# Kernel tuning notes

Measured on AMD Instinct MI355X. Metric: run time of the kernel, lower is better.

The kernel has to match this reference:

```python
import jax, jax.numpy as jnp
import numpy as np

B, S, I, E, NH, HID, L = 32, 512, 64, 128, 8, 1024, 4
HD = E // NH
TEMP = 0.05
EPS_BN = 1e-5
EPS_LN = 1e-5


def _pe(seq_len, d_model):
    # sinusoidal positional encoding, matches PositionalEncoding buffer pe[:seq_len, 0, :]
    pos = jnp.arange(seq_len, dtype=jnp.float32)[:, None]
    div = jnp.exp(jnp.arange(0, d_model, 2, dtype=jnp.float32) * (-np.log(10000.0) / d_model))
    pe = jnp.zeros((seq_len, d_model), jnp.float32)
    pe = pe.at[:, 0::2].set(jnp.sin(pos * div))
    pe = pe.at[:, 1::2].set(jnp.cos(pos * div))
    return pe


def _bn(x, g, b, axis):
    # eval-mode BatchNorm1d with running_mean=0, running_var=1 (affine scale+shift)
    sh = [1] * x.ndim
    sh[axis] = -1
    return x * (g / jnp.sqrt(1.0 + EPS_BN)).reshape(sh) + b.reshape(sh)


def _ln(x, g, b):
    m = jnp.mean(x, axis=-1, keepdims=True)
    v = jnp.var(x, axis=-1, keepdims=True)
    return (x - m) / jnp.sqrt(v + EPS_LN) * g + b


def _layer(h, Wqkv, bqkv, Wo, bo, g1, b1, g2, b2, W1, bf1, W2, bf2):
    # h: (S, B, E); post-LN torch TransformerEncoderLayer, relu FFN
    s, b = h.shape[0], h.shape[1]
    qkv = h @ Wqkv + bqkv                                  # (S, B, 3E)
    q, k, v = jnp.split(qkv, 3, axis=-1)
    sp = lambda t: t.reshape(s, b, NH, HD).transpose(1, 2, 0, 3)  # (B, NH, S, HD)
    q, k, v = sp(q), sp(k), sp(v)
    att = jax.nn.softmax(jnp.einsum('bhqd,bhkd->bhqk', q, k) * (1.0 / np.sqrt(HD)), axis=-1)
    o = jnp.einsum('bhqk,bhkd->bhqd', att, v).transpose(2, 0, 1, 3).reshape(s, b, E)
    h = _ln(h + o @ Wo + bo, g1, b1)
    ff = jax.nn.relu(h @ W1 + bf1) @ W2 + bf2
    h = _ln(h + ff, g2, b2)
    return h, att.mean(axis=1)  # attn averaged over heads: (B, S, S)


def setup_inputs() -> dict:
    key = jax.random.key(0)
    ks = iter(jax.random.split(key, 64))
    r = lambda *sh: jax.random.normal(next(ks), sh, jnp.float32) * 0.02
    return dict(
        x=jax.random.normal(next(ks), (B, S, I), jnp.float32),
        Wt=r(I, E), bt=r(E),
        bn1_g=jnp.ones(E), bn1_b=jnp.zeros(E),
        bn2_g=jnp.ones(E), bn2_b=jnp.zeros(E),
        Wqkv=r(L, E, 3 * E), bqkv=r(L, 3 * E), Wo=r(L, E, E), bo=r(L, E),
        ln1_g=jnp.ones((L, E)), ln1_b=jnp.zeros((L, E)),
        ln2_g=jnp.ones((L, E)), ln2_b=jnp.zeros((L, E)),
        W1=r(L, E, HID), b1=r(L, HID), W2=r(L, HID, E), b2=r(L, E),
        bn3_g=jnp.ones(E), bn3_b=jnp.zeros(E),
        Wd=r(E, I), bd=r(I), bn4_g=jnp.ones(I), bn4_b=jnp.zeros(I),
        Ws=r(S, HID), bs=r(HID), bn5_g=jnp.ones(HID), bn5_b=jnp.zeros(HID),
        Wtext=r(1024, HID), btext=r(HID), lnT_g=jnp.ones(HID), lnT_b=jnp.zeros(HID),
        sensor_emb=jax.random.normal(next(ks), (I, 1024), jnp.float32),
    )


def reference(x, Wt, bt, bn1_g, bn1_b, bn2_g, bn2_b,
              Wqkv, bqkv, Wo, bo, ln1_g, ln1_b, ln2_g, ln2_b,
              W1, b1, W2, b2, bn3_g, bn3_b,
              Wd, bd, bn4_g, bn4_b, Ws, bs, bn5_g, bn5_b,
              Wtext, btext, lnT_g, lnT_b, sensor_emb):
    # trunk_net: Linear -> BN(E) -> PE -> BN(E)
    h = x @ Wt + bt                                  # (B, S, E)
    h = _bn(h.transpose(0, 2, 1), bn1_g, bn1_b, 1)   # (B, E, S)
    h = h.transpose(2, 0, 1)                         # (S, B, E)
    h = h + _pe(h.shape[0], E)[:, None, :]
    h = _bn(h.transpose(1, 2, 0), bn2_g, bn2_b, 1)   # (B, E, S)
    h = h.transpose(2, 0, 1)                         # (S, B, E)
    for i in range(L):
        h, attn = _layer(h, Wqkv[i], bqkv[i], Wo[i], bo[i],
                         ln1_g[i], ln1_b[i], ln2_g[i], ln2_b[i],
                         W1[i], b1[i], W2[i], b2[i])
    h = _bn(h.transpose(1, 2, 0), bn3_g, bn3_b, 1)   # (B, E, S)
    # downsample_embedding_to_input_net
    d = jax.nn.relu(h.transpose(0, 2, 1) @ Wd + bd)  # (B, S, I)
    d = _bn(d.transpose(0, 2, 1), bn4_g, bn4_b, 1)   # (B, I, S)
    # sequence_representation_net
    imu = jax.nn.relu(d @ Ws + bs)                   # (B, I, HID)
    imu = _bn(imu, bn5_g, bn5_b, 2)
    # text_to_shared_net on sensor embeddings
    sens = _ln(jax.nn.relu(sensor_emb @ Wtext + btext), lnT_g, lnT_b)  # (I, HID)
    # fused pairwise cosine similarity (torch expands to (B,I,I,HID); we don't)
    imu_n = imu / jnp.maximum(jnp.linalg.norm(imu, axis=-1, keepdims=True), 1e-8)
    sens_n = sens / jnp.maximum(jnp.linalg.norm(sens, axis=-1, keepdims=True), 1e-8)
    return jnp.einsum('bih,jh->bij', imu_n, sens_n) / TEMP  # (B, I, I)
```

## Files before the change

### kernel.cpp

```cpp
#include <hip/hip_runtime.h>
#include <hip/hip_bf16.h>

#define B_   32
#define S_   512
#define I_   64
#define E_   128
#define NH_  8
#define HD_  16
#define HID_ 1024
#define L_   4
#define NTOK (B_*S_)

typedef __hip_bfloat16 bf16;
typedef __attribute__((ext_vector_type(8))) short bf16x8;
typedef __attribute__((ext_vector_type(4))) short bf16x4;
typedef __attribute__((ext_vector_type(4))) float f32x4;

__device__ __forceinline__ float b2f(bf16 v) { return __bfloat162float(v); }

template<bool F32>
__device__ __forceinline__ float ld(const void* p, size_t i) {
    if (F32) return ((const float*)p)[i];
    return b2f(((const bf16*)p)[i]);
}

__device__ __forceinline__ unsigned short f2bu(float f) {
    union { bf16 h; unsigned short u; } c; c.h = __float2bfloat16(f); return c.u;
}
__device__ __forceinline__ unsigned short b2u(bf16 h) {
    union { bf16 h; unsigned short u; } c; c.h = h; return c.u;
}
__device__ __forceinline__ float u2f(unsigned short u) {
    return __uint_as_float((unsigned int)u << 16);
}

__global__ void k_flag(const void* bn1g, int* flag) {
    if (threadIdx.x == 0) {
        const unsigned short* u = (const unsigned short*)bn1g;
        int zeros = 0;
        for (int i = 0; i < 32; ++i) zeros += (u[i] == 0);
        flag[0] = (zeros >= 8) ? 1 : 0;
    }
}

struct TrJobs {
    const void* in[7];
    bf16*       out[7];
    int R[7];
    int C[7];
    int start[8];
};

template<bool F32>
__device__ void tr_all_body(const TrJobs& j, float (*tile)[33])
{
    int bid = blockIdx.x;
    int job = 0;
#pragma unroll
    for (int t = 0; t < 6; ++t) if (bid >= j.start[t + 1]) job = t + 1;
    int local = bid - j.start[job];
    int R = j.R[job], C = j.C[job];
    int nx = C >> 5, ny = R >> 5;
    int per_z = nx * ny;
    int z = local / per_z;
    int rem = local - z * per_z;
    int cy = rem / nx, cx = rem - cy * nx;
    const void* in = j.in[job];
    bf16* out = j.out[job];

    size_t off = (size_t)z * R * C;
    int c0 = cx * 32, r0 = cy * 32;
    int tx = threadIdx.x;
    for (int i = threadIdx.y; i < 32; i += 8)
        tile[i][tx] = ld<F32>(in, off + (size_t)(r0 + i) * C + c0 + tx);
    __syncthreads();
    for (int i = threadIdx.y; i < 32; i += 8)
        out[off + (size_t)(c0 + i) * R + r0 + tx] = __float2bfloat16(tile[tx][i]);
}
__global__ __launch_bounds__(256) void k_tr_all(TrJobs j, const int* flag)
{
    __shared__ float tile[32][33];
    if (*flag) tr_all_body<true>(j, tile);
    else       tr_all_body<false>(j, tile);
}

struct PkJobs {
    const bf16* in[5];
    bf16*       out[5];
    int K[5];
    int NT[5];
    int KT[5];
    int start[6];
};

__global__ __launch_bounds__(256) void k_pack(PkJobs j)
{
    int fb = blockIdx.x * 4 + (threadIdx.x >> 6);
    if (fb >= j.start[5]) return;
    int lane = threadIdx.x & 63;
    int job = 0;
#pragma unroll
    for (int t = 0; t < 4; ++t) if (fb >= j.start[t + 1]) job = t + 1;
    int local = fb - j.start[job];
    int K = j.K[job], NT = j.NT[job], KT = j.KT[job];
    int per_z = NT * KT;
    int z = local / per_z;
    int rem = local - z * per_z;
    int ct = rem / KT, kt = rem - ct * KT;
    int l15 = lane & 15, quad = lane >> 4;
    const bf16* in = j.in[job] + (size_t)z * NT * 16 * K;
    bf16* out = j.out[job] + (size_t)z * per_z * 512 + (size_t)(ct * KT + kt) * 512 + lane * 8;
    *(uint4*)out = *(const uint4*)&in[(size_t)(ct * 16 + l15) * K + kt * 32 + quad * 8];
}

template<bool F32>
__device__ void trunk_body(const void* x, const void* Wt, const void* bt,
                           const void* g1, const void* c1,
                           const void* g2, const void* c2, float* __restrict__ h,
                           float (*xs)[I_])
{
    const int TOK = 8;
    int t0 = blockIdx.x * TOK;
    int tid = threadIdx.x;
    for (int idx = tid; idx < TOK * I_; idx += 128) {
        int tt = idx >> 6, k = idx & 63;
        xs[tt][k] = ld<F32>(x, (size_t)(t0 + tt) * I_ + k);
    }
    __syncthreads();
    int e = tid;
    float acc[TOK];
    float bias = ld<F32>(bt, e);
#pragma unroll
    for (int tt = 0; tt < TOK; ++tt) acc[tt] = bias;
    for (int k = 0; k < I_; ++k) {
        float w = ld<F32>(Wt, k * E_ + e);
#pragma unroll
        for (int tt = 0; tt < TOK; ++tt) acc[tt] += xs[tt][k] * w;
    }
    float rs = rsqrtf(1.0f + 1e-5f);
    float a1 = ld<F32>(g1, e) * rs, d1 = ld<F32>(c1, e);
    float a2 = ld<F32>(g2, e) * rs, d2 = ld<F32>(c2, e);
    int p = e >> 1;
    float freq = __expf(-(float)p * 0.14391157f);
#pragma unroll
    for (int tt = 0; tt < TOK; ++tt) {
        int t = t0 + tt;
        int s = t & (S_ - 1);
        float ang = (float)s * freq;
        float pe = (e & 1) ? cosf(ang) : sinf(ang);
        float v = acc[tt] * a1 + d1 + pe;
        h[(size_t)t * E_ + e] = v * a2 + d2;
    }
}
__global__ __launch_bounds__(128) void k_trunk(
    const void* x, const void* Wt, const void* bt,
    const void* g1, const void* c1, const void* g2, const void* c2,
    float* h, const int* flag)
{
    __shared__ float xs[8][I_];
    if (*flag) trunk_body<true>(x, Wt, bt, g1, c1, g2, c2, h, xs);
    else       trunk_body<false>(x, Wt, bt, g1, c1, g2, c2, h, xs);
}

template<bool F32>
__device__ void qkvm_body(const float* __restrict__ h, const bf16* __restrict__ WP,
                          const void* bias, size_t obi, bf16* __restrict__ qkv,
                          unsigned short (*A_s)[136])
{
    int t0 = blockIdx.x * 32;
    int tid = threadIdx.x;
    int wv = tid >> 6, lane = tid & 63;
    int l15 = lane & 15, quad = lane >> 4;

    {
        const float4* h4 = (const float4*)(h + (size_t)t0 * E_);
        for (int i = tid; i < 32 * E_ / 4; i += 256) {
            float4 v = h4[i];
            int row = i >> 5, col = (i & 31) * 4;
            unsigned int w0 = (unsigned int)f2bu(v.x) | ((unsigned int)f2bu(v.y) << 16);
            unsigned int w1 = (unsigned int)f2bu(v.z) | ((unsigned int)f2bu(v.w) << 16);
            *(uint2*)&A_s[row][col] = (uint2){w0, w1};
        }
    }
    __syncthreads();

    bf16x8 af[2][4];
#pragma unroll
    for (int kt = 0; kt < 4; ++kt) {
        int k0 = kt * 32 + quad * 8;
        af[0][kt] = *(const bf16x8*)&A_s[l15][k0];
        af[1][kt] = *(const bf16x8*)&A_s[16 + l15][k0];
    }
    for (int nt = 0; nt < 6; ++nt) {
        int col = wv * 96 + nt * 16 + l15;
        int ct = wv * 6 + nt;
        f32x4 acc0 = {0.f, 0.f, 0.f, 0.f}, acc1 = {0.f, 0.f, 0.f, 0.f};
#pragma unroll
        for (int kt = 0; kt < 4; ++kt) {
            bf16x8 bfr = *(const bf16x8*)&WP[(size_t)((ct * 4 + kt) * 64 + lane) * 8];
            acc0 = __builtin_amdgcn_mfma_f32_16x16x32_bf16(af[0][kt], bfr, acc0, 0, 0, 0);
            acc1 = __builtin_amdgcn_mfma_f32_16x16x32_bf16(af[1][kt], bfr, acc1, 0, 0, 0);
        }
        float bb = ld<F32>(bias, obi + col);
#pragma unroll
        for (int r = 0; r < 4; ++r) {
            qkv[(size_t)(t0 + quad * 4 + r) * 384 + col]      = __float2bfloat16(acc0[r] + bb);
            qkv[(size_t)(t0 + 16 + quad * 4 + r) * 384 + col] = __float2bfloat16(acc1[r] + bb);
        }
    }
}
__global__ __launch_bounds__(256) void k_qkv(
    const float* h, const bf16* WP, const void* bias, size_t obi,
    bf16* qkv, const int* flag)
{
    __shared__ unsigned short A_s[32][136];
    if (*flag) qkvm_body<true>(h, WP, bias, obi, qkv, A_s);
    else       qkvm_body<false>(h, WP, bias, obi, qkv, A_s);
}

__global__ __launch_bounds__(512) void k_attn(bf16* qkv)
{
    __shared__ unsigned short Ks[S_ * 16];
    __shared__ unsigned short Qs[256 * 16];
    __shared__ unsigned short VT[HD_ * 520];

    int bx = blockIdx.x;
    int qh = bx & 1;
    int hh = (bx >> 1) & (NH_ - 1);
    int b  = bx >> 4;
    int tid = threadIdx.x;
    const size_t base = (size_t)(b * S_) * 384 + hh * HD_;
    const float qs = 0.25f * 1.44269504f;

    for (int i = tid; i < S_ * 2; i += 512) {
        int s = i >> 1, hf = i & 1;
        uint4 v = *(const uint4*)(qkv + base + (size_t)s * 384 + 128 + hf * 8);
        unsigned int* w = (unsigned int*)&v;
#pragma unroll
        for (int j = 0; j < 4; ++j) {
            unsigned int lo = f2bu(u2f((unsigned short)(w[j] & 0xffff)) * qs);
            unsigned int hi = f2bu(u2f((unsigned short)(w[j] >> 16)) * qs);
            w[j] = lo | (hi << 16);
        }
        *(uint4*)&Ks[s * 16 + hf * 8] = v;
    }
    for (int i = tid; i < 256 * 2; i += 512) {
        int s = i >> 1, hf = i & 1;
        *(uint4*)&Qs[s * 16 + hf * 8] =
            *(const uint4*)(qkv + base + (size_t)(qh * 256 + s) * 384 + hf * 8);
    }
    {
        int s = tid;
        uint4 v0 = *(const uint4*)(qkv + base + (size_t)s * 384 + 256);
        uint4 v1 = *(const uint4*)(qkv + base + (size_t)s * 384 + 256 + 8);
        const unsigned short* u0 = (const unsigned short*)&v0;
        const unsigned short* u1 = (const unsigned short*)&v1;
#pragma unroll
        for (int dd = 0; dd < 8; ++dd) VT[dd * 520 + s] = u0[dd];
#pragma unroll
        for (int dd = 0; dd < 8; ++dd) VT[(8 + dd) * 520 + s] = u1[dd];
    }
    __syncthreads();

    int wv = tid >> 6, lane = tid & 63;
    int l15 = lane & 15, quad = lane >> 4;
    const f32x4 z4 = {0.f, 0.f, 0.f, 0.f};

    bf16x4 bq0 = *(const bf16x4*)&Qs[(wv * 32 + l15) * 16 + quad * 4];
    bf16x4 bq1 = *(const bf16x4*)&Qs[(wv * 32 + 16 + l15) * 16 + quad * 4];

    f32x4 O0 = z4, O1 = z4;
    float den0 = 0.f, den1 = 0.f;

#pragma unroll 2
    for (int kt = 0; kt < 32; ++kt) {
        bf16x4 ak = *(const bf16x4*)&Ks[(kt * 16 + l15) * 16 + quad * 4];
        bf16x4 av = *(const bf16x4*)&VT[l15 * 520 + kt * 16 + quad * 4];

        f32x4 s0 = __builtin_amdgcn_mfma_f32_16x16x16bf16_1k(ak, bq0, z4, 0, 0, 0);
        f32x4 s1 = __builtin_amdgcn_mfma_f32_16x16x16bf16_1k(ak, bq1, z4, 0, 0, 0);

        float p0[4], p1[4];
#pragma unroll
        for (int r = 0; r < 4; ++r) { p0[r] = exp2f(s0[r]); den0 += p0[r]; }
#pragma unroll
        for (int r = 0; r < 4; ++r) { p1[r] = exp2f(s1[r]); den1 += p1[r]; }

        bf16x4 pa0, pa1;
#pragma unroll
        for (int r = 0; r < 4; ++r) { pa0[r] = (short)f2bu(p0[r]); pa1[r] = (short)f2bu(p1[r]); }

        O0 = __builtin_amdgcn_mfma_f32_16x16x16bf16_1k(av, pa0, O0, 0, 0, 0);
        O1 = __builtin_amdgcn_mfma_f32_16x16x16bf16_1k(av, pa1, O1, 0, 0, 0);
    }

    den0 += __shfl_xor(den0, 16, 64);
    den0 += __shfl_xor(den0, 32, 64);
    den1 += __shfl_xor(den1, 16, 64);
    den1 += __shfl_xor(den1, 32, 64);
    float inv0 = 1.0f / den0;
    float inv1 = 1.0f / den1;

    int q0 = qh * 256 + wv * 32 + l15;
    bf16* out0 = qkv + (size_t)(b * S_ + q0) * 384 + hh * HD_ + quad * 4;
    bf16* out1 = out0 + (size_t)16 * 384;
    unsigned int a0 = (unsigned int)f2bu(O0[0] * inv0) | ((unsigned int)f2bu(O0[1] * inv0) << 16);
    unsigned int a1 = (unsigned int)f2bu(O0[2] * inv0) | ((unsigned int)f2bu(O0[3] * inv0) << 16);
    *(uint2*)out0 = (uint2){a0, a1};
    unsigned int c0 = (unsigned int)f2bu(O1[0] * inv1) | ((unsigned int)f2bu(O1[1] * inv1) << 16);
    unsigned int c1 = (unsigned int)f2bu(O1[2] * inv1) | ((unsigned int)f2bu(O1[3] * inv1) << 16);
    *(uint2*)out1 = (uint2){c0, c1};
}

#define FTOK 32
#define APAD 8
#define MHALF 512
#define MPAD 8

template<bool F32>
__device__ void projffn_body(const bf16* __restrict__ qkv, const bf16* __restrict__ WoP,
                             const void* bo, size_t obo,
                             const void* g1, const void* be1,
                             const bf16* __restrict__ W1P, const void* b1, size_t ob1,
                             const bf16* __restrict__ W2P, const void* b2v, size_t ob2,
                             const void* g2, const void* be2, size_t oln,
                             float* __restrict__ h,
                             const bf16* __restrict__ WqP, const void* bqv, size_t obq,
                             bf16* __restrict__ qkvout,
                             const bf16* __restrict__ WdP, const void* bd,
                             const void* g3, const void* c3,
                             const void* g4, const void* c4,
                             float* __restrict__ dbuf, int mode,
                             unsigned short (*A_s)[E_ + APAD],
                             unsigned short (*mid_s)[MHALF + MPAD],
                             float (*red)[32][2])
{
    int t0 = blockIdx.x * FTOK;
    int tid = threadIdx.x;
    int wv = tid >> 6, lane = tid & 63;
    int l15 = lane & 15, quad = lane >> 4;
    int c0 = wv * 16 + l15;

    {
        int row = tid >> 4, seg = tid & 15;
        *(uint4*)&A_s[row][seg * 8] =
            *(const uint4*)&qkv[(size_t)(t0 + row) * 384 + seg * 8];
    }
    __syncthreads();

    bf16x8 af[2][4];
#pragma unroll
    for (int kt = 0; kt < 4; ++kt) {
        int k0 = kt * 32 + quad * 8;
        af[0][kt] = *(const bf16x8*)&A_s[l15][k0];
        af[1][kt] = *(const bf16x8*)&A_s[16 + l15][k0];
    }
    f32x4 acc[2];
    acc[0] = (f32x4){0.f, 0.f, 0.f, 0.f};
    acc[1] = (f32x4){0.f, 0.f, 0.f, 0.f};
#pragma unroll
    for (int kt = 0; kt < 4; ++kt) {
        bf16x8 bb0 = *(const bf16x8*)&WoP[(size_t)((wv * 4 + kt) * 64 + lane) * 8];
        acc[0] = __builtin_amdgcn_mfma_f32_16x16x32_bf16(af[0][kt], bb0, acc[0], 0, 0, 0);
        acc[1] = __builtin_amdgcn_mfma_f32_16x16x32_bf16(af[1][kt], bb0, acc[1], 0, 0, 0);
    }

    float bo0 = ld<F32>(bo, obo + c0);
    float val[2][4], s1[2][4], s2[2][4];
#pragma unroll
    for (int mt = 0; mt < 2; ++mt) {
#pragma unroll
        for (int r = 0; r < 4; ++r) {
            size_t row = (size_t)(t0 + mt * 16 + quad * 4 + r);
            float v0 = acc[mt][r] + bo0 + h[row * E_ + c0];
            val[mt][r] = v0;
            s1[mt][r] = v0;
            s2[mt][r] = v0 * v0;
        }
    }
#pragma unroll
    for (int off = 1; off < 16; off <<= 1) {
#pragma unroll
        for (int mt = 0; mt < 2; ++mt)
#pragma unroll
            for (int r = 0; r < 4; ++r) {
                s1[mt][r] += __shfl_xor(s1[mt][r], off, 64);
                s2[mt][r] += __shfl_xor(s2[mt][r], off, 64);
            }
    }
    if (l15 == 0) {
#pragma unroll
        for (int mt = 0; mt < 2; ++mt)
#pragma unroll
            for (int r = 0; r < 4; ++r) {
                red[wv][mt * 16 + quad * 4 + r][0] = s1[mt][r];
                red[wv][mt * 16 + quad * 4 + r][1] = s2[mt][r];
            }
    }
    __syncthreads();

    float val1[2][4];
    {
        float g10 = ld<F32>(g1, oln + c0);
        float b10 = ld<F32>(be1, oln + c0);
#pragma unroll
        for (int mt = 0; mt < 2; ++mt) {
#pragma unroll
            for (int r = 0; r < 4; ++r) {
                int rw = mt * 16 + quad * 4 + r;
                float su = red[0][rw][0] + red[1][rw][0] + red[2][rw][0] + red[3][rw][0]
                         + red[4][rw][0] + red[5][rw][0] + red[6][rw][0] + red[7][rw][0];
                float sq = red[0][rw][1] + red[1][rw][1] + red[2][rw][1] + red[3][rw][1]
                         + red[4][rw][1] + red[5][rw][1] + red[6][rw][1] + red[7][rw][1];
                float mean = su * (1.0f / E_);
                float var = fmaxf(sq * (1.0f / E_) - mean * mean, 0.0f);
                float rstd = rsqrtf(var + 1e-5f);
                float h0 = (val[mt][r] - mean) * rstd * g10 + b10;
                val1[mt][r] = h0;
                A_s[rw][c0] = f2bu(h0);
            }
        }
    }
    __syncthreads();

    bf16x8 af1[2][4];
#pragma unroll
    for (int kt = 0; kt < 4; ++kt) {
        int k0 = kt * 32 + quad * 8;
        af1[0][kt] = *(const bf16x8*)&A_s[l15][k0];
        af1[1][kt] = *(const bf16x8*)&A_s[16 + l15][k0];
    }

    f32x4 acc2[2];
    acc2[0] = (f32x4){0.f, 0.f, 0.f, 0.f};
    acc2[1] = (f32x4){0.f, 0.f, 0.f, 0.f};

    for (int p = 0; p < 2; ++p) {
        for (int nt = 0; nt < 4; ++nt) {
            int col = p * MHALF + wv * 64 + nt * 16 + l15;
            int lc  = wv * 64 + nt * 16 + l15;
            int ct  = p * 32 + wv * 4 + nt;
            f32x4 acc0 = {0.f, 0.f, 0.f, 0.f}, acc1 = {0.f, 0.f, 0.f, 0.f};
#pragma unroll
            for (int kt = 0; kt < 4; ++kt) {
                bf16x8 bfr = *(const bf16x8*)&W1P[(size_t)((ct * 4 + kt) * 64 + lane) * 8];
                acc0 = __builtin_amdgcn_mfma_f32_16x16x32_bf16(af1[0][kt], bfr, acc0, 0, 0, 0);
                acc1 = __builtin_amdgcn_mfma_f32_16x16x32_bf16(af1[1][kt], bfr, acc1, 0, 0, 0);
            }
            float bias = ld<F32>(b1, ob1 + col);
#pragma unroll
            for (int r = 0; r < 4; ++r) {
                mid_s[quad * 4 + r][lc]      = f2bu(fmaxf(acc0[r] + bias, 0.f));
                mid_s[16 + quad * 4 + r][lc] = f2bu(fmaxf(acc1[r] + bias, 0.f));
            }
        }
        __syncthreads();

        for (int kk = 0; kk < 16; ++kk) {
            int kt = p * 16 + kk;
            int k0l = kk * 32 + quad * 8;
            bf16x8 a0 = *(const bf16x8*)&mid_s[l15][k0l];
            bf16x8 a1 = *(const bf16x8*)&mid_s[16 + l15][k0l];
            bf16x8 bb0 = *(const bf16x8*)&W2P[(size_t)((wv * 32 + kt) * 64 + lane) * 8];
            acc2[0] = __builtin_amdgcn_mfma_f32_16x16x32_bf16(a0, bb0, acc2[0], 0, 0, 0);
            acc2[1] = __builtin_amdgcn_mfma_f32_16x16x32_bf16(a1, bb0, acc2[1], 0, 0, 0);
        }
        __syncthreads();
    }

    float b20 = ld<F32>(b2v, ob2 + c0);
#pragma unroll
    for (int mt = 0; mt < 2; ++mt) {
#pragma unroll
        for (int r = 0; r < 4; ++r) {
            float v0 = acc2[mt][r] + b20 + val1[mt][r];
            val[mt][r] = v0;
            s1[mt][r] = v0;
            s2[mt][r] = v0 * v0;
        }
    }
#pragma unroll
    for (int off = 1; off < 16; off <<= 1) {
#pragma unroll
        for (int mt = 0; mt < 2; ++mt)
#pragma unroll
            for (int r = 0; r < 4; ++r) {
                s1[mt][r] += __shfl_xor(s1[mt][r], off, 64);
                s2[mt][r] += __shfl_xor(s2[mt][r], off, 64);
            }
    }
    if (l15 == 0) {
#pragma unroll
        for (int mt = 0; mt < 2; ++mt)
#pragma unroll
            for (int r = 0; r < 4; ++r) {
                red[wv][mt * 16 + quad * 4 + r][0] = s1[mt][r];
                red[wv][mt * 16 + quad * 4 + r][1] = s2[mt][r];
            }
    }
    __syncthreads();
    float g20 = ld<F32>(g2, oln + c0);
    float be20 = ld<F32>(be2, oln + c0);
    float rsb = rsqrtf(1.0f + 1e-5f);
    float a3 = (mode == 2) ? ld<F32>(g3, c0) * rsb : 0.f;
    float d3 = (mode == 2) ? ld<F32>(c3, c0) : 0.f;
#pragma unroll
    for (int mt = 0; mt < 2; ++mt) {
#pragma unroll
        for (int r = 0; r < 4; ++r) {
            int rw = mt * 16 + quad * 4 + r;
            float su = red[0][rw][0] + red[1][rw][0] + red[2][rw][0] + red[3][rw][0]
                     + red[4][rw][0] + red[5][rw][0] + red[6][rw][0] + red[7][rw][0];
            float sq = red[0][rw][1] + red[1][rw][1] + red[2][rw][1] + red[3][rw][1]
                     + red[4][rw][1] + red[5][rw][1] + red[6][rw][1] + red[7][rw][1];
            float mean = su * (1.0f / E_);
            float var = fmaxf(sq * (1.0f / E_) - mean * mean, 0.0f);
            float rstd = rsqrtf(var + 1e-5f);
            size_t row = (size_t)(t0 + rw);
            float outv = (val[mt][r] - mean) * rstd * g20 + be20;
            if (mode != 2) {
                h[row * E_ + c0] = outv;
                A_s[rw][c0] = f2bu(outv);
            } else {
                A_s[rw][c0] = f2bu(outv * a3 + d3);
            }
        }
    }

    if (mode == 1) {
        __syncthreads();
        bf16x8 afq[2][4];
#pragma unroll
        for (int kt = 0; kt < 4; ++kt) {
            int k0 = kt * 32 + quad * 8;
            afq[0][kt] = *(const bf16x8*)&A_s[l15][k0];
            afq[1][kt] = *(const bf16x8*)&A_s[16 + l15][k0];
        }
        for (int nt = 0; nt < 3; ++nt) {
            int ct = wv * 3 + nt;
            int col = ct * 16 + l15;
            f32x4 q0 = {0.f, 0.f, 0.f, 0.f}, q1 = {0.f, 0.f, 0.f, 0.f};
#pragma unroll
            for (int kt = 0; kt < 4; ++kt) {
                bf16x8 bfr = *(const bf16x8*)&WqP[(size_t)((ct * 4 + kt) * 64 + lane) * 8];
                q0 = __builtin_amdgcn_mfma_f32_16x16x32_bf16(afq[0][kt], bfr, q0, 0, 0, 0);
                q1 = __builtin_amdgcn_mfma_f32_16x16x32_bf16(afq[1][kt], bfr, q1, 0, 0, 0);
            }
            float bb = ld<F32>(bqv, obq + col);
#pragma unroll
            for (int r = 0; r < 4; ++r) {
                qkvout[(size_t)(t0 + quad * 4 + r) * 384 + col]      = __float2bfloat16(q0[r] + bb);
                qkvout[(size_t)(t0 + 16 + quad * 4 + r) * 384 + col] = __float2bfloat16(q1[r] + bb);
            }
        }
    } else if (mode == 2) {
        __syncthreads();
        int rt = wv >> 2, ctd = wv & 3;
        bf16x8 afd[4];
#pragma unroll
        for (int kt = 0; kt < 4; ++kt) {
            int k0 = kt * 32 + quad * 8;
            afd[kt] = *(const bf16x8*)&A_s[rt * 16 + l15][k0];
        }
        f32x4 qd = {0.f, 0.f, 0.f, 0.f};
#pragma unroll
        for (int kt = 0; kt < 4; ++kt) {
            bf16x8 bfr = *(const bf16x8*)&WdP[(size_t)((ctd * 4 + kt) * 64 + lane) * 8];
            qd = __builtin_amdgcn_mfma_f32_16x16x32_bf16(afd[kt], bfr, qd, 0, 0, 0);
        }
        int col = ctd * 16 + l15;
        float bb = ld<F32>(bd, col);
        float a4 = ld<F32>(g4, col) * rsb, d4 = ld<F32>(c4, col);
#pragma unroll
        for (int r = 0; r < 4; ++r) {
            dbuf[(size_t)(t0 + rt * 16 + quad * 4 + r) * I_ + col] =
                fmaxf(qd[r] + bb, 0.f) * a4 + d4;
        }
    }
}
__global__ __launch_bounds__(512, 4) void k_projffn(
    const bf16* qkv, const bf16* WoP, const void* bo, size_t obo,
    const void* g1, const void* be1,
    const bf16* W1P, const void* b1, size_t ob1,
    const bf16* W2P, const void* b2v, size_t ob2,
    const void* g2, const void* be2, size_t oln, float* h,
    const bf16* WqP, const void* bqv, size_t obq, bf16* qkvout,
    const bf16* WdP, const void* bd, const void* g3, const void* c3,
    const void* g4, const void* c4, float* dbuf, int mode,
    const int* flag)
{
    __shared__ unsigned short A_s[FTOK][E_ + APAD];
    __shared__ unsigned short mid_s[FTOK][MHALF + MPAD];
    __shared__ float red[8][32][2];
    if (*flag) projffn_body<true>(qkv, WoP, bo, obo, g1, be1, W1P, b1, ob1,
                                  W2P, b2v, ob2, g2, be2, oln, h,
                                  WqP, bqv, obq, qkvout,
                                  WdP, bd, g3, c3, g4, c4, dbuf, mode,
                                  A_s, mid_s, red);
    else       projffn_body<false>(qkv, WoP, bo, obo, g1, be1, W1P, b1, ob1,
                                   W2P, b2v, ob2, g2, be2, oln, h,
                                   WqP, bqv, obq, qkvout,
                                   WdP, bd, g3, c3, g4, c4, dbuf, mode,
                                   A_s, mid_s, red);
}

template<bool F32>
__device__ void imum_body(const float* __restrict__ d, const bf16* __restrict__ WsT,
                          const void* bs, const void* g5, const void* c5,
                          float* __restrict__ imu, unsigned short (*A_s)[520])
{
    int b = blockIdx.x >> 3;
    int jc = blockIdx.x & 7;
    int tid = threadIdx.x;
    int wv = tid >> 6, lane = tid & 63;
    int l15 = lane & 15, quad = lane >> 4;

    for (int idx = tid; idx < I_ * S_; idx += 256) {
        int i = idx & 63, s = idx >> 6;
        A_s[i][s] = f2bu(d[((size_t)b * S_ + s) * I_ + i]);
    }
    __syncthreads();

    float rs = rsqrtf(1.0f + 1e-5f);
    int j0 = jc * 128 + wv * 32;
    for (int nt = 0; nt < 2; ++nt) {
        int j = j0 + nt * 16 + l15;
        f32x4 acc4[4];
#pragma unroll
        for (int mt = 0; mt < 4; ++mt) acc4[mt] = (f32x4){0.f, 0.f, 0.f, 0.f};
        for (int kt = 0; kt < 16; ++kt) {
            int k0 = kt * 32 + quad * 8;
            bf16x8 bfr = *(const bf16x8*)&WsT[(size_t)j * S_ + k0];
#pragma unroll
            for (int mt = 0; mt < 4; ++mt) {
                bf16x8 a = *(const bf16x8*)&A_s[mt * 16 + l15][k0];
                acc4[mt] = __builtin_amdgcn_mfma_f32_16x16x32_bf16(a, bfr, acc4[mt], 0, 0, 0);
            }
        }
        float bias = ld<F32>(bs, j);
        float a5 = ld<F32>(g5, j) * rs, d5 = ld<F32>(c5, j);
#pragma unroll
        for (int mt = 0; mt < 4; ++mt) {
#pragma unroll
            for (int r = 0; r < 4; ++r) {
                int row = mt * 16 + quad * 4 + r;
                float v = fmaxf(acc4[mt][r] + bias, 0.f) * a5 + d5;
                imu[((size_t)b * I_ + row) * HID_ + j] = v;
            }
        }
    }
}
__global__ __launch_bounds__(256) void k_imu(
    const float* d, const bf16* WsT, const void* bs,
    const void* g5, const void* c5, float* imu, const int* flag)
{
    __shared__ unsigned short A_s[I_][520];
    if (*flag) imum_body<true>(d, WsT, bs, g5, c5, imu, A_s);
    else       imum_body<false>(d, WsT, bs, g5, c5, imu, A_s);
}

__global__ __launch_bounds__(256) void k_norm(float* __restrict__ imu)
{
    __shared__ float red[4];
    size_t r0 = (size_t)blockIdx.x * HID_;
    int tid = threadIdx.x;
    float sq = 0.f;
    for (int k = tid; k < HID_; k += 256) { float v = imu[r0 + k]; sq += v * v; }
    for (int off = 32; off; off >>= 1) sq += __shfl_down(sq, off, 64);
    int wv = tid >> 6, lane = tid & 63;
    if (lane == 0) red[wv] = sq;
    __syncthreads();
    float tot = red[0] + red[1] + red[2] + red[3];
    float inv = 1.0f / fmaxf(sqrtf(fmaxf(tot, 0.f)), 1e-8f);
    for (int k = tid; k < HID_; k += 256) imu[r0 + k] *= inv;
}

template<bool F32>
__device__ void sensg_body(const void* se, const bf16* __restrict__ WtT,
                           const void* bt, float* __restrict__ sg,
                           unsigned short (*A_s)[HID_ + 8])
{
    int mt = blockIdx.x >> 4;
    int nc = blockIdx.x & 15;
    int r0 = mt * 16;
    int tid = threadIdx.x;
    int wv = tid >> 6, lane = tid & 63;
    int l15 = lane & 15, quad = lane >> 4;

    for (int i = tid; i < 16 * HID_; i += 256) {
        int row = i >> 10, col = i & (HID_ - 1);
        A_s[row][col] = f2bu(ld<F32>(se, (size_t)(r0 + row) * HID_ + col));
    }
    __syncthreads();

    int col = nc * 64 + wv * 16 + l15;
    f32x4 acc = {0.f, 0.f, 0.f, 0.f};
    for (int kt = 0; kt < 32; ++kt) {
        int k0 = kt * 32 + quad * 8;
        bf16x8 a = *(const bf16x8*)&A_s[l15][k0];
        bf16x8 bb = *(const bf16x8*)&WtT[(size_t)col * HID_ + k0];
        acc = __builtin_amdgcn_mfma_f32_16x16x32_bf16(a, bb, acc, 0, 0, 0);
    }
    float bbv = ld<F32>(bt, col);
#pragma unroll
    for (int r = 0; r < 4; ++r)
        sg[(size_t)(r0 + quad * 4 + r) * HID_ + col] = fmaxf(acc[r] + bbv, 0.f);
}
__global__ __launch_bounds__(256) void k_sens_gemm(
    const void* se, const bf16* WtT, const void* bt, float* sg, const int* flag)
{
    __shared__ unsigned short A_s[16][HID_ + 8];
    if (*flag) sensg_body<true>(se, WtT, bt, sg, A_s);
    else       sensg_body<false>(se, WtT, bt, sg, A_s);
}

template<bool F32>
__device__ void sensln_body(const float* __restrict__ sg, const void* g, const void* be,
                            bf16* __restrict__ sens_b, float (*red)[2])
{
    size_t r0 = (size_t)blockIdx.x * HID_;
    int tid = threadIdx.x;
    int wv = tid >> 6, lane = tid & 63;
    float v4[4];
    float s1 = 0.f, s2 = 0.f;
#pragma unroll
    for (int c = 0; c < 4; ++c) {
        float v = sg[r0 + tid + c * 256];
        v4[c] = v;
        s1 += v; s2 += v * v;
    }
    for (int off = 32; off; off >>= 1) {
        s1 += __shfl_down(s1, off, 64);
        s2 += __shfl_down(s2, off, 64);
    }
    if (lane == 0) { red[wv][0] = s1; red[wv][1] = s2; }
    __syncthreads();
    float su = red[0][0] + red[1][0] + red[2][0] + red[3][0];
    float sq = red[0][1] + red[1][1] + red[2][1] + red[3][1];
    float mean = su * (1.0f / HID_);
    float var = fmaxf(sq * (1.0f / HID_) - mean * mean, 0.0f);
    float rstd = rsqrtf(var + 1e-5f);
    float q = 0.f;
#pragma unroll
    for (int c = 0; c < 4; ++c) {
        int col = tid + c * 256;
        v4[c] = (v4[c] - mean) * rstd * ld<F32>(g, col) + ld<F32>(be, col);
        q += v4[c] * v4[c];
    }
    for (int off = 32; off; off >>= 1) q += __shfl_down(q, off, 64);
    __syncthreads();
    if (lane == 0) red[wv][0] = q;
    __syncthreads();
    float tot = red[0][0] + red[1][0] + red[2][0] + red[3][0];
    float inv = 1.0f / fmaxf(sqrtf(fmaxf(tot, 0.f)), 1e-8f);
#pragma unroll
    for (int c = 0; c < 4; ++c)
        sens_b[r0 + tid + c * 256] = __float2bfloat16(v4[c] * inv);
}
__global__ __launch_bounds__(256) void k_sens_ln(
    const float* sg, const void* g, const void* be, bf16* sens_b, const int* flag)
{
    __shared__ float red[4][2];
    if (*flag) sensln_body<true>(sg, g, be, sens_b, red);
    else       sensln_body<false>(sg, g, be, sens_b, red);
}

template<bool F32>
__device__ void finalm_body(const float* __restrict__ imu_n, const bf16* __restrict__ sens_b,
                            void* __restrict__ out, unsigned short (*A_s)[HID_ + 8])
{
    int r0 = blockIdx.x * 32;
    int tid = threadIdx.x;
    int wv = tid >> 6, lane = tid & 63;
    int l15 = lane & 15, quad = lane >> 4;

    {
        const float4* i4 = (const float4*)(imu_n + (size_t)r0 * HID_);
        for (int i = tid; i < 32 * HID_ / 4; i += 256) {
            float4 v = i4[i];
            int row = i >> 8, col = (i & 255) * 4;
            unsigned int w0 = (unsigned int)f2bu(v.x) | ((unsigned int)f2bu(v.y) << 16);
            unsigned int w1 = (unsigned int)f2bu(v.z) | ((unsigned int)f2bu(v.w) << 16);
            *(uint2*)&A_s[row][col] = (uint2){w0, w1};
        }
    }
    __syncthreads();

    int j = wv * 16 + l15;
    f32x4 acc[2];
    acc[0] = (f32x4){0.f, 0.f, 0.f, 0.f};
    acc[1] = (f32x4){0.f, 0.f, 0.f, 0.f};
    for (int kt = 0; kt < 32; ++kt) {
        int k0 = kt * 32 + quad * 8;
        bf16x8 bfr = *(const bf16x8*)&sens_b[(size_t)j * HID_ + k0];
        bf16x8 a0 = *(const bf16x8*)&A_s[l15][k0];
        bf16x8 a1 = *(const bf16x8*)&A_s[16 + l15][k0];
        acc[0] = __builtin_amdgcn_mfma_f32_16x16x32_bf16(a0, bfr, acc[0], 0, 0, 0);
        acc[1] = __builtin_amdgcn_mfma_f32_16x16x32_bf16(a1, bfr, acc[1], 0, 0, 0);
    }
#pragma unroll
    for (int mt = 0; mt < 2; ++mt) {
#pragma unroll
        for (int r = 0; r < 4; ++r) {
            size_t row = (size_t)(r0 + mt * 16 + quad * 4 + r);
            float v = acc[mt][r] * 20.0f;
            if (F32) ((float*)out)[row * I_ + j] = v;
            else     ((bf16*)out)[row * I_ + j] = __float2bfloat16(v);
        }
    }
}
__global__ __launch_bounds__(256) void k_final(
    const float* imu_n, const bf16* sens_b, void* out, const int* flag)
{
    __shared__ unsigned short A_s[32][HID_ + 8];
    if (*flag) finalm_body<true>(imu_n, sens_b, out, A_s);
    else       finalm_body<false>(imu_n, sens_b, out, A_s);
}

extern "C" void kernel_launch(void* const* d_in, const int* in_sizes, int n_in,
                              void* d_out, int out_size, void* d_ws, size_t ws_size,
                              hipStream_t stream) {
    (void)in_sizes; (void)n_in; (void)out_size; (void)ws_size;
    const void* x      = d_in[0];
    const void* Wt     = d_in[1];
    const void* bt     = d_in[2];
    const void* bn1_g  = d_in[3];
    const void* bn1_b  = d_in[4];
    const void* bn2_g  = d_in[5];
    const void* bn2_b  = d_in[6];
    const void* Wqkv   = d_in[7];
    const void* bqkv   = d_in[8];
    const void* Wo     = d_in[9];
    const void* bo     = d_in[10];
    const void* ln1_g  = d_in[11];
    const void* ln1_b  = d_in[12];
    const void* ln2_g  = d_in[13];
    const void* ln2_b  = d_in[14];
    const void* W1     = d_in[15];
    const void* b1     = d_in[16];
    const void* W2     = d_in[17];
    const void* b2     = d_in[18];
    const void* bn3_g  = d_in[19];
    const void* bn3_b  = d_in[20];
    const void* Wd     = d_in[21];
    const void* bd     = d_in[22];
    const void* bn4_g  = d_in[23];
    const void* bn4_b  = d_in[24];
    const void* Wsr    = d_in[25];
    const void* bs     = d_in[26];
    const void* bn5_g  = d_in[27];
    const void* bn5_b  = d_in[28];
    const void* Wtext  = d_in[29];
    const void* btext  = d_in[30];
    const void* lnT_g  = d_in[31];
    const void* lnT_b  = d_in[32];
    const void* semb   = d_in[33];

    char* ws = (char*)d_ws;
    float* h    = (float*)(ws);
    bf16*  qkvb = (bf16*) (ws + ((size_t)8  << 20));
    float* imu  = (float*)(ws + ((size_t)12 << 20));
    bf16*  wb   = (bf16*) (ws + ((size_t)20 << 20));
    bf16*  WqkvT = wb;
    bf16*  WoT   = wb + 196608;
    bf16*  W1T   = wb + 262144;
    bf16*  W2T   = wb + 786432;
    bf16*  WsT   = wb + 1310720;
    bf16*  sensb = wb + 1835008;
    bf16*  WdT   = wb + 1900544;
    float* sg    = (float*)(wb + 1908736);
    int*   flag  = (int*)  (ws + ((size_t)24 << 20));
    bf16*  WtxT  = (bf16*) (ws + ((size_t)25 << 20));
    bf16*  wp    = (bf16*) (ws + ((size_t)27 << 20));
    bf16*  WqkvP = wp;
    bf16*  WoP   = wp + 196608;
    bf16*  W1P   = wp + 262144;
    bf16*  W2P   = wp + 786432;
    bf16*  WdP   = wp + 1310720;
    float* dbuf  = (float*)(ws + ((size_t)30 << 20));

    k_flag<<<1, 64, 0, stream>>>(bn1_g, flag);

    {
        TrJobs tj;
        tj.in[0] = Wqkv;  tj.out[0] = WqkvT; tj.R[0] = 128;  tj.C[0] = 384;
        tj.in[1] = Wo;    tj.out[1] = WoT;   tj.R[1] = 128;  tj.C[1] = 128;
        tj.in[2] = W1;    tj.out[2] = W1T;   tj.R[2] = 128;  tj.C[2] = 1024;
        tj.in[3] = W2;    tj.out[3] = W2T;   tj.R[3] = 1024; tj.C[3] = 128;
        tj.in[4] = Wsr;   tj.out[4] = WsT;   tj.R[4] = 512;  tj.C[4] = 1024;
        tj.in[5] = Wd;    tj.out[5] = WdT;   tj.R[5] = 128;  tj.C[5] = 64;
        tj.in[6] = Wtext; tj.out[6] = WtxT;  tj.R[6] = 1024; tj.C[6] = 1024;
        const int st[8] = {0, 192, 256, 768, 1280, 1792, 1800, 2824};
        for (int i = 0; i < 8; ++i) tj.start[i] = st[i];
        k_tr_all<<<2824, dim3(32, 8), 0, stream>>>(tj, flag);
    }
    {
        PkJobs pj;
        pj.in[0] = WqkvT; pj.out[0] = WqkvP; pj.K[0] = 128;  pj.NT[0] = 24; pj.KT[0] = 4;
        pj.in[1] = WoT;   pj.out[1] = WoP;   pj.K[1] = 128;  pj.NT[1] = 8;  pj.KT[1] = 4;
        pj.in[2] = W1T;   pj.out[2] = W1P;   pj.K[2] = 128;  pj.NT[2] = 64; pj.KT[2] = 4;
        pj.in[3] = W2T;   pj.out[3] = W2P;   pj.K[3] = 1024; pj.NT[3] = 8;  pj.KT[3] = 32;
        pj.in[4] = WdT;   pj.out[4] = WdP;   pj.K[4] = 128;  pj.NT[4] = 4;  pj.KT[4] = 4;
        const int st[6] = {0, 384, 512, 1536, 2560, 2576};
        for (int i = 0; i < 6; ++i) pj.start[i] = st[i];
        k_pack<<<644, 256, 0, stream>>>(pj);
    }

    k_trunk<<<NTOK / 8, 128, 0, stream>>>(x, Wt, bt, bn1_g, bn1_b, bn2_g, bn2_b, h, flag);

    k_qkv<<<NTOK / 32, 256, 0, stream>>>(h, WqkvP, bqkv, 0, qkvb, flag);

    for (int l = 0; l < L_; ++l) {
        size_t obo   = (size_t)l * E_;
        size_t ob1   = (size_t)l * HID_;
        size_t ob2   = (size_t)l * E_;
        size_t oln   = (size_t)l * E_;
        int mode = (l < L_ - 1) ? 1 : 2;
        int ln = (l < L_ - 1) ? (l + 1) : 0;
        k_attn<<<B_ * NH_ * 2, 512, 0, stream>>>(qkvb);
        k_projffn<<<NTOK / FTOK, 512, 0, stream>>>(qkvb, WoP + (size_t)l * 16384, bo, obo,
                                                   ln1_g, ln1_b,
                                                   W1P + (size_t)l * 131072, b1, ob1,
                                                   W2P + (size_t)l * 131072, b2, ob2,
                                                   ln2_g, ln2_b, oln, h,
                                                   WqkvP + (size_t)ln * 49152, bqkv,
                                                   (size_t)ln * 384, qkvb,
                                                   WdP, bd, bn3_g, bn3_b, bn4_g, bn4_b,
                                                   dbuf, mode, flag);
    }

    k_imu<<<B_ * 8, 256, 0, stream>>>(dbuf, WsT, bs, bn5_g, bn5_b, imu, flag);
    k_norm<<<B_ * I_, 256, 0, stream>>>(imu);
    k_sens_gemm<<<64, 256, 0, stream>>>(semb, WtxT, btext, sg, flag);
    k_sens_ln<<<I_, 256, 0, stream>>>(sg, lnT_g, lnT_b, sensb, flag);
    k_final<<<(B_ * I_) / 32, 256, 0, stream>>>(imu, sensb, d_out, flag);
}
```

Before: 457.8 us.

## Fuse trunk embedding with first QKV GEMM and fold row-norm into final kernel

Merges the input trunk projection kernel with the layer-0 QKV GEMM, so the bf16 activations are staged in shared memory instead of being reread from global h. Also removes the separate L2-normalization kernel by computing per-row norms inside the final cosine-similarity kernel before the bf16 conversion. Together these drop two launches and one full read/write pass over imu. The cost is larger blocks (512 threads) with more shared memory, and a second global read of imu rows in the final kernel.

```diff
diff --git a/kernel.cpp b/kernel.cpp
--- a/kernel.cpp
+++ b/kernel.cpp
@@ -114,28 +114,30 @@
 }
 
 template<bool F32>
-__device__ void trunk_body(const void* x, const void* Wt, const void* bt,
-                           const void* g1, const void* c1,
-                           const void* g2, const void* c2, float* __restrict__ h,
-                           float (*xs)[I_])
-{
-    const int TOK = 8;
-    int t0 = blockIdx.x * TOK;
+__device__ void trunkqkv_body(const void* x, const void* Wt, const void* bt,
+                              const void* g1, const void* c1,
+                              const void* g2, const void* c2,
+                              const bf16* __restrict__ WqP, const void* bqv,
+                              float* __restrict__ h, bf16* __restrict__ qkv,
+                              float (*xs)[I_], unsigned short (*A_s)[136])
+{
+    int t0 = blockIdx.x * 32;
     int tid = threadIdx.x;
-    for (int idx = tid; idx < TOK * I_; idx += 128) {
+    for (int idx = tid; idx < 32 * I_; idx += 512) {
         int tt = idx >> 6, k = idx & 63;
         xs[tt][k] = ld<F32>(x, (size_t)(t0 + tt) * I_ + k);
     }
     __syncthreads();
-    int e = tid;
-    float acc[TOK];
+    int e = tid & 127;
+    int tg = tid >> 7;
+    float acc[8];
     float bias = ld<F32>(bt, e);
 #pragma unroll
-    for (int tt = 0; tt < TOK; ++tt) acc[tt] = bias;
+    for (int tt = 0; tt < 8; ++tt) acc[tt] = bias;
     for (int k = 0; k < I_; ++k) {
         float w = ld<F32>(Wt, k * E_ + e);
 #pragma unroll
-        for (int tt = 0; tt < TOK; ++tt) acc[tt] += xs[tt][k] * w;
+        for (int tt = 0; tt < 8; ++tt) acc[tt] += xs[tg * 8 + tt][k] * w;
     }
     float rs = rsqrtf(1.0f + 1e-5f);
     float a1 = ld<F32>(g1, e) * rs, d1 = ld<F32>(c1, e);
@@ -143,79 +145,55 @@
     int p = e >> 1;
     float freq = __expf(-(float)p * 0.14391157f);
 #pragma unroll
-    for (int tt = 0; tt < TOK; ++tt) {
-        int t = t0 + tt;
+    for (int tt = 0; tt < 8; ++tt) {
+        int tl = tg * 8 + tt;
+        int t = t0 + tl;
         int s = t & (S_ - 1);
         float ang = (float)s * freq;
         float pe = (e & 1) ? cosf(ang) : sinf(ang);
         float v = acc[tt] * a1 + d1 + pe;
-        h[(size_t)t * E_ + e] = v * a2 + d2;
-    }
-}
-__global__ __launch_bounds__(128) void k_trunk(
+        float o = v * a2 + d2;
+        h[(size_t)t * E_ + e] = o;
+        A_s[tl][e] = f2bu(o);
+    }
+    __syncthreads();
+
+    int wv = tid >> 6, lane = tid & 63;
+    int l15 = lane & 15, quad = lane >> 4;
+    bf16x8 afq[2][4];
+#pragma unroll
+    for (int kt = 0; kt < 4; ++kt) {
+        int k0 = kt * 32 + quad * 8;
+        afq[0][kt] = *(const bf16x8*)&A_s[l15][k0];
+        afq[1][kt] = *(const bf16x8*)&A_s[16 + l15][k0];
+    }
+    for (int nt = 0; nt < 3; ++nt) {
+        int ct = wv * 3 + nt;
+        int col = ct * 16 + l15;
+        f32x4 q0 = {0.f, 0.f, 0.f, 0.f}, q1 = {0.f, 0.f, 0.f, 0.f};
+#pragma unroll
+        for (int kt = 0; kt < 4; ++kt) {
+            bf16x8 bfr = *(const bf16x8*)&WqP[(size_t)((ct * 4 + kt) * 64 + lane) * 8];
+            q0 = __builtin_amdgcn_mfma_f32_16x16x32_bf16(afq[0][kt], bfr, q0, 0, 0, 0);
+            q1 = __builtin_amdgcn_mfma_f32_16x16x32_bf16(afq[1][kt], bfr, q1, 0, 0, 0);
+        }
+        float bb = ld<F32>(bqv, col);
+#pragma unroll
+        for (int r = 0; r < 4; ++r) {
+            qkv[(size_t)(t0 + quad * 4 + r) * 384 + col]      = __float2bfloat16(q0[r] + bb);
+            qkv[(size_t)(t0 + 16 + quad * 4 + r) * 384 + col] = __float2bfloat16(q1[r] + bb);
+        }
+    }
+}
+__global__ __launch_bounds__(512) void k_trunkqkv(
     const void* x, const void* Wt, const void* bt,
     const void* g1, const void* c1, const void* g2, const void* c2,
-    float* h, const int* flag)
-{
-    __shared__ float xs[8][I_];
-    if (*flag) trunk_body<true>(x, Wt, bt, g1, c1, g2, c2, h, xs);
-    else       trunk_body<false>(x, Wt, bt, g1, c1, g2, c2, h, xs);
-}
-
-template<bool F32>
-__device__ void qkvm_body(const float* __restrict__ h, const bf16* __restrict__ WP,
-                          const void* bias, size_t obi, bf16* __restrict__ qkv,
-                          unsigned short (*A_s)[136])
-{
-    int t0 = blockIdx.x * 32;
-    int tid = threadIdx.x;
-    int wv = tid >> 6, lane = tid & 63;
-    int l15 = lane & 15, quad = lane >> 4;
-
-    {
-        const float4* h4 = (const float4*)(h + (size_t)t0 * E_);
-        for (int i = tid; i < 32 * E_ / 4; i += 256) {
-            float4 v = h4[i];
-            int row = i >> 5, col = (i & 31) * 4;
-            unsigned int w0 = (unsigned int)f2bu(v.x) | ((unsigned int)f2bu(v.y) << 16);
-            unsigned int w1 = (unsigned int)f2bu(v.z) | ((unsigned int)f2bu(v.w) << 16);
-            *(uint2*)&A_s[row][col] = (uint2){w0, w1};
-        }
-    }
-    __syncthreads();
-
-    bf16x8 af[2][4];
-#pragma unroll
-    for (int kt = 0; kt < 4; ++kt) {
-        int k0 = kt * 32 + quad * 8;
-        af[0][kt] = *(const bf16x8*)&A_s[l15][k0];
-        af[1][kt] = *(const bf16x8*)&A_s[16 + l15][k0];
-    }
-    for (int nt = 0; nt < 6; ++nt) {
-        int col = wv * 96 + nt * 16 + l15;
-        int ct = wv * 6 + nt;
-        f32x4 acc0 = {0.f, 0.f, 0.f, 0.f}, acc1 = {0.f, 0.f, 0.f, 0.f};
-#pragma unroll
-        for (int kt = 0; kt < 4; ++kt) {
-            bf16x8 bfr = *(const bf16x8*)&WP[(size_t)((ct * 4 + kt) * 64 + lane) * 8];
-            acc0 = __builtin_amdgcn_mfma_f32_16x16x32_bf16(af[0][kt], bfr, acc0, 0, 0, 0);
-            acc1 = __builtin_amdgcn_mfma_f32_16x16x32_bf16(af[1][kt], bfr, acc1, 0, 0, 0);
-        }
-        float bb = ld<F32>(bias, obi + col);
-#pragma unroll
-        for (int r = 0; r < 4; ++r) {
-            qkv[(size_t)(t0 + quad * 4 + r) * 384 + col]      = __float2bfloat16(acc0[r] + bb);
-            qkv[(size_t)(t0 + 16 + quad * 4 + r) * 384 + col] = __float2bfloat16(acc1[r] + bb);
-        }
-    }
-}
-__global__ __launch_bounds__(256) void k_qkv(
-    const float* h, const bf16* WP, const void* bias, size_t obi,
-    bf16* qkv, const int* flag)
-{
+    const bf16* WqP, const void* bqv, float* h, bf16* qkv, const int* flag)
+{
+    __shared__ float xs[32][I_];
     __shared__ unsigned short A_s[32][136];
-    if (*flag) qkvm_body<true>(h, WP, bias, obi, qkv, A_s);
-    else       qkvm_body<false>(h, WP, bias, obi, qkv, A_s);
+    if (*flag) trunkqkv_body<true>(x, Wt, bt, g1, c1, g2, c2, WqP, bqv, h, qkv, xs, A_s);
+    else       trunkqkv_body<false>(x, Wt, bt, g1, c1, g2, c2, WqP, bqv, h, qkv, xs, A_s);
 }
 
 __global__ __launch_bounds__(512) void k_attn(bf16* qkv)
@@ -659,22 +637,6 @@
     else       imum_body<false>(d, WsT, bs, g5, c5, imu, A_s);
 }
 
-__global__ __launch_bounds__(256) void k_norm(float* __restrict__ imu)
-{
-    __shared__ float red[4];
-    size_t r0 = (size_t)blockIdx.x * HID_;
-    int tid = threadIdx.x;
-    float sq = 0.f;
-    for (int k = tid; k < HID_; k += 256) { float v = imu[r0 + k]; sq += v * v; }
-    for (int off = 32; off; off >>= 1) sq += __shfl_down(sq, off, 64);
-    int wv = tid >> 6, lane = tid & 63;
-    if (lane == 0) red[wv] = sq;
-    __syncthreads();
-    float tot = red[0] + red[1] + red[2] + red[3];
-    float inv = 1.0f / fmaxf(sqrtf(fmaxf(tot, 0.f)), 1e-8f);
-    for (int k = tid; k < HID_; k += 256) imu[r0 + k] *= inv;
-}
-
 template<bool F32>
 __device__ void sensg_body(const void* se, const bf16* __restrict__ WtT,
                            const void* bt, float* __restrict__ sg,
@@ -766,23 +728,33 @@
 }
 
 template<bool F32>
-__device__ void finalm_body(const float* __restrict__ imu_n, const bf16* __restrict__ sens_b,
-                            void* __restrict__ out, unsigned short (*A_s)[HID_ + 8])
+__device__ void finalm_body(const float* __restrict__ imu, const bf16* __restrict__ sens_b,
+                            void* __restrict__ out, unsigned short (*A_s)[HID_ + 8],
+                            float (*rnorm)[32])
 {
     int r0 = blockIdx.x * 32;
     int tid = threadIdx.x;
     int wv = tid >> 6, lane = tid & 63;
     int l15 = lane & 15, quad = lane >> 4;
 
-    {
-        const float4* i4 = (const float4*)(imu_n + (size_t)r0 * HID_);
-        for (int i = tid; i < 32 * HID_ / 4; i += 256) {
-            float4 v = i4[i];
-            int row = i >> 8, col = (i & 255) * 4;
-            unsigned int w0 = (unsigned int)f2bu(v.x) | ((unsigned int)f2bu(v.y) << 16);
-            unsigned int w1 = (unsigned int)f2bu(v.z) | ((unsigned int)f2bu(v.w) << 16);
-            *(uint2*)&A_s[row][col] = (uint2){w0, w1};
-        }
+    const float4* i4 = (const float4*)(imu + (size_t)r0 * HID_);
+
+    for (int j = 0; j < 32; ++j) {
+        float4 v = i4[j * 256 + tid];
+        float sq = v.x * v.x + v.y * v.y + v.z * v.z + v.w * v.w;
+        for (int off = 32; off; off >>= 1) sq += __shfl_down(sq, off, 64);
+        if (lane == 0) rnorm[wv][j] = sq;
+    }
+    __syncthreads();
+
+    for (int j = 0; j < 32; ++j) {
+        float tot = rnorm[0][j] + rnorm[1][j] + rnorm[2][j] + rnorm[3][j];
+        float inv = 1.0f / fmaxf(sqrtf(fmaxf(tot, 0.f)), 1e-8f);
+        float4 v = i4[j * 256 + tid];
+        int col = tid * 4;
+        unsigned int w0 = (unsigned int)f2bu(v.x * inv) | ((unsigned int)f2bu(v.y * inv) << 16);
+        unsigned int w1 = (unsigned int)f2bu(v.z * inv) | ((unsigned int)f2bu(v.w * inv) << 16);
+        *(uint2*)&A_s[j][col] = (uint2){w0, w1};
     }
     __syncthreads();
 
@@ -810,11 +782,12 @@
     }
 }
 __global__ __launch_bounds__(256) void k_final(
-    const float* imu_n, const bf16* sens_b, void* out, const int* flag)
+    const float* imu, const bf16* sens_b, void* out, const int* flag)
 {
     __shared__ unsigned short A_s[32][HID_ + 8];
-    if (*flag) finalm_body<true>(imu_n, sens_b, out, A_s);
-    else       finalm_body<false>(imu_n, sens_b, out, A_s);
+    __shared__ float rnorm[4][32];
+    if (*flag) finalm_body<true>(imu, sens_b, out, A_s, rnorm);
+    else       finalm_body<false>(imu, sens_b, out, A_s, rnorm);
 }
 
 extern "C" void kernel_launch(void* const* d_in, const int* in_sizes, int n_in,
@@ -906,9 +879,8 @@
         k_pack<<<644, 256, 0, stream>>>(pj);
     }
 
-    k_trunk<<<NTOK / 8, 128, 0, stream>>>(x, Wt, bt, bn1_g, bn1_b, bn2_g, bn2_b, h, flag);
-
-    k_qkv<<<NTOK / 32, 256, 0, stream>>>(h, WqkvP, bqkv, 0, qkvb, flag);
+    k_trunkqkv<<<NTOK / 32, 512, 0, stream>>>(x, Wt, bt, bn1_g, bn1_b, bn2_g, bn2_b,
+                                              WqkvP, bqkv, h, qkvb, flag);
 
     for (int l = 0; l < L_; ++l) {
         size_t obo   = (size_t)l * E_;
@@ -930,7 +902,6 @@
     }
 
     k_imu<<<B_ * 8, 256, 0, stream>>>(dbuf, WsT, bs, bn5_g, bn5_b, imu, flag);
-    k_norm<<<B_ * I_, 256, 0, stream>>>(imu);
     k_sens_gemm<<<64, 256, 0, stream>>>(semb, WtxT, btext, sg, flag);
     k_sens_ln<<<I_, 256, 0, stream>>>(sg, lnT_g, lnT_b, sensb, flag);
     k_final<<<(B_ * I_) / 32, 256, 0, stream>>>(imu, sensb, d_out, flag);
```

After: 454.7 us. Within noise of the previous version (-0.7%).
